# Optimization experiments

Hardware: AMD Instinct MI355X
Metric: run time of the kernel (lower is better)

## Reference

```python
import jax, jax.numpy as jnp
import numpy as np
from jax import lax

NH = 4          # num_head
DIM = 512       # attention dim
VDIM = 512      # v_dim
QDIM = 1024     # q_dim
KS = 100        # loc_kernel_size -> conv width 2*KS+1
KN = 100        # loc_kernel_num
TEMP = 0.5      # temperature
BS, TS = 8, 2048


def setup_inputs() -> dict:
    key = jax.random.key(0)
    ks = jax.random.split(key, 12)
    s = 0.05
    return {
        "dec_state": jax.random.normal(ks[0], (BS, QDIM), jnp.float32),
        "enc_feat": jax.random.normal(ks[1], (BS, TS, VDIM), jnp.float32),
        "enc_len": jax.random.randint(ks[2], (BS,), TS // 2, TS + 1).astype(jnp.int32),
        "Wq": jax.random.normal(ks[3], (NH * DIM, QDIM), jnp.float32) * s,
        "bq": jnp.zeros((NH * DIM,), jnp.float32),
        "Wk": jax.random.normal(ks[4], (NH * DIM, VDIM), jnp.float32) * s,
        "bk": jnp.zeros((NH * DIM,), jnp.float32),
        "Wv": jax.random.normal(ks[5], (NH * VDIM, VDIM), jnp.float32) * s,
        "bv": jnp.zeros((NH * VDIM,), jnp.float32),
        "loc_conv_w": jax.random.normal(ks[6], (KN, NH, 2 * KS + 1), jnp.float32) * s,
        "loc_proj_w": jax.random.normal(ks[7], (DIM, KN), jnp.float32) * s,
        "gen_w": jax.random.normal(ks[8], (1, DIM), jnp.float32) * s,
        "gen_b": jnp.zeros((1,), jnp.float32),
        "merge_w": jax.random.normal(ks[9], (VDIM, NH * VDIM), jnp.float32) * s,
        "merge_b": jnp.zeros((VDIM,), jnp.float32),
    }


def reference(dec_state, enc_feat, enc_len, Wq, bq, Wk, bk, Wv, bv,
              loc_conv_w, loc_proj_w, gen_w, gen_b, merge_w, merge_b):
    bs, ts, _ = enc_feat.shape
    # query: [bs, nh, dim]
    query = jnp.tanh(dec_state @ Wq.T + bq).reshape(bs, NH, DIM)
    # key/value: [bs, nh, ts, dim]/[bs, nh, ts, v_dim]
    key = jnp.tanh(enc_feat @ Wk.T + bk).reshape(bs, ts, NH, DIM).transpose(0, 2, 1, 3)
    value = jnp.tanh(enc_feat @ Wv.T + bv).reshape(bs, ts, NH, VDIM).transpose(0, 2, 1, 3)
    # mask & initial (uniform-over-valid) previous attention
    pos = jnp.arange(ts)
    pad_mask = pos[None, :] >= enc_len[:, None]                      # [bs, ts] True = padded
    prev = jnp.where(pad_mask, 0.0, 1.0 / enc_len[:, None].astype(jnp.float32))  # [bs, ts]
    prev_att = jnp.broadcast_to(prev[:, None, :], (bs, NH, ts))      # [bs, nh, ts]
    # location features: Conv1d(nh -> kn, width 2*KS+1, pad KS, no bias)
    conv = lax.conv_general_dilated(prev_att, loc_conv_w, (1,), [(KS, KS)],
                                    dimension_numbers=("NCH", "OIH", "NCH"))  # [bs, kn, ts]
    loc = jnp.tanh(jnp.einsum("bkt,dk->btd", conv, loc_proj_w))      # [bs, ts, dim]
    # additive energy: gen_energy(tanh(k + q + loc))
    e = jnp.tanh(key + query[:, :, None, :] + loc[:, None, :, :])    # [bs, nh, ts, dim]
    energy = jnp.einsum("bhtd,d->bht", e, gen_w[0]) + gen_b[0]
    energy = energy / TEMP
    energy = jnp.where(pad_mask[:, None, :], -jnp.inf, energy)
    attn = jax.nn.softmax(energy, axis=-1)                           # [bs, nh, ts]
    ctx = jnp.einsum("bht,bhtv->bhv", attn, value).reshape(bs, NH * VDIM)
    context = ctx @ merge_w.T + merge_b                              # [bs, v_dim]
    return attn, context
```

## Files before the change

kernel.cpp:

```cpp
#include <hip/hip_runtime.h>
#include <math.h>

#define NH 4
#define DIM 512
#define VDIM 512
#define QDIM 1024
#define KS 100
#define KN 100
#define TEMPERATURE 0.5f
#define BS 8
#define TS 2048
#define NHD (NH * DIM)

#define WS_QUERY  0
#define WS_QTAB   16384
#define WS_ENERGY 119808
#define WS_CTX    185344
#define WS_LOCI   201728
#define WS_P      205824
#define WS_F32_END 226028

typedef __bf16 bf16x8 __attribute__((ext_vector_type(8)));
typedef __bf16 bf16x4 __attribute__((ext_vector_type(4)));
typedef float  f32x4  __attribute__((ext_vector_type(4)));

#define AS1(p) ((const __attribute__((address_space(1))) void*)(p))
#define AS3(p) ((__attribute__((address_space(3))) void*)(p))

__device__ __forceinline__ float fast_tanh(float x) {
    float xc = fminf(fmaxf(x, -9.0f), 9.0f);
    float e = __expf(2.0f * xc);
    return __fdividef(e - 1.0f, e + 1.0f);
}

#define NE4 (BS * TS * VDIM / 4)
#define NW4 (NHD * VDIM / 4)
__global__ void k_cvt3(const float* __restrict__ enc, const float* __restrict__ Wk,
                       const float* __restrict__ Wv, __bf16* __restrict__ enc_bf,
                       __bf16* __restrict__ wk_bf, __bf16* __restrict__ wv_bf) {
    int i = blockIdx.x * blockDim.x + threadIdx.x;
    const float* src; __bf16* dst; int k;
    if (i < NE4)                { src = enc; dst = enc_bf; k = i; }
    else if (i < NE4 + NW4)     { src = Wk;  dst = wk_bf;  k = i - NE4; }
    else                        { src = Wv;  dst = wv_bf;  k = i - NE4 - NW4; }
    float4 v = ((const float4*)src)[k];
    bf16x4 o;
    o[0] = (__bf16)v.x; o[1] = (__bf16)v.y; o[2] = (__bf16)v.z; o[3] = (__bf16)v.w;
    ((bf16x4*)dst)[k] = o;
}

__global__ void k_query(const float* __restrict__ dec, const float* __restrict__ Wq,
                        const float* __restrict__ bq, float* __restrict__ query) {
    int w = (blockIdx.x * blockDim.x + threadIdx.x) >> 6;
    int lane = threadIdx.x & 63;
    int b = w >> 11;
    int o = w & 2047;
    const float* dr = dec + b * QDIM;
    const float* wr = Wq + o * QDIM;
    float s = 0.f;
    #pragma unroll
    for (int i = 0; i < QDIM / 64; ++i) s = fmaf(dr[lane + 64 * i], wr[lane + 64 * i], s);
    #pragma unroll
    for (int off = 32; off > 0; off >>= 1) s += __shfl_down(s, off);
    if (lane == 0) query[b * NHD + o] = tanhf(s + bq[o]);
}

__global__ void k_prefix(const float* __restrict__ convw, float* __restrict__ P) {
    int k = threadIdx.x;
    if (k >= KN) return;
    const float* wr = convw + k * (NH * (2 * KS + 1));
    float acc = 0.f;
    P[k] = 0.f;
    for (int dt = 0; dt < 2 * KS + 1; ++dt) {
        acc += wr[dt] + wr[201 + dt] + wr[402 + dt] + wr[603 + dt];
        P[(dt + 1) * KN + k] = acc;
    }
}

__global__ void k_qtab(const float* __restrict__ P, const float* __restrict__ projw,
                       float* __restrict__ Qtab) {
    int j = blockIdx.x;
    __shared__ float Pc[KN];
    int tid = threadIdx.x;
    if (tid < KN) Pc[tid] = P[j * KN + tid];
    __syncthreads();
    const float* pr = projw + tid * KN;
    float s = 0.f;
    #pragma unroll 4
    for (int k = 0; k < KN; ++k) s = fmaf(pr[k], Pc[k], s);
    Qtab[j * DIM + tid] = s;
}

__global__ void k_locI(const float* __restrict__ Qtab, const int* __restrict__ enc_len,
                       float* __restrict__ locI) {
    int idx = blockIdx.x * blockDim.x + threadIdx.x;
    int b = idx >> 9, d = idx & (DIM - 1);
    float inv_len = 1.0f / (float)enc_len[b];
    locI[idx] = fast_tanh((Qtab[(2 * KS + 1) * DIM + d] - Qtab[d]) * inv_len);
}

#define STAGE2(AshB, BshB, k0)                                                    \
    {                                                                             \
        int cch = (lane & 7) ^ (lane >> 3);                                       \
        _Pragma("unroll")                                                         \
        for (int q = 0; q < 2; ++q) {                                             \
            int slotbase = (w * 2 + q) * 64;                                      \
            int m = (slotbase >> 3) + (lane >> 3);                                \
            __builtin_amdgcn_global_load_lds(                                     \
                AS1(Abase + (size_t)m * VDIM + (k0) + cch * 8),                   \
                AS3((AshB) + slotbase * 8), 16, 0, 0);                            \
            __builtin_amdgcn_global_load_lds(                                     \
                AS1(Bbase + (size_t)m * VDIM + (k0) + cch * 8),                   \
                AS3((BshB) + slotbase * 8), 16, 0, 0);                            \
        }                                                                         \
    }

#define GEMM_MAIN(Bglobal, EARLY)                                                 \
    const int t0 = blockIdx.x * 128;                                              \
    const int n0 = blockIdx.y * 128;                                              \
    const int b  = blockIdx.z;                                                    \
    EARLY                                                                         \
    const int tid = threadIdx.x;                                                  \
    const int w = tid >> 6, lane = tid & 63;                                      \
    const int wy = w >> 2, wx = w & 3;                                            \
    const int col = lane & 15, quad = lane >> 4;                                  \
    __shared__ __bf16 Ash[2][128 * 64];                                           \
    __shared__ __bf16 Bsh[2][128 * 64];                                           \
    f32x4 acc[4][2];                                                              \
    _Pragma("unroll")                                                             \
    for (int i = 0; i < 4; ++i)                                                   \
        _Pragma("unroll")                                                         \
        for (int j = 0; j < 2; ++j) acc[i][j] = (f32x4)0.f;                       \
    const __bf16* Abase = enc_bf + ((size_t)b * TS + t0) * VDIM;                  \
    const __bf16* Bbase = (Bglobal) + (size_t)n0 * VDIM;                          \
    STAGE2(Ash[0], Bsh[0], 0)                                                     \
    for (int kk = 0; kk < 8; ++kk) {                                              \
        __syncthreads();                                                          \
        if (kk < 7) STAGE2(Ash[(kk + 1) & 1], Bsh[(kk + 1) & 1], (kk + 1) * 64)   \
        const __bf16* As = Ash[kk & 1];                                           \
        const __bf16* Bs = Bsh[kk & 1];                                           \
        _Pragma("unroll")                                                         \
        for (int ks = 0; ks < 2; ++ks) {                                          \
            bf16x8 af[4], bfr[2];                                                 \
            int jslot = ((ks * 4 + quad) ^ (col & 7));                            \
            _Pragma("unroll")                                                     \
            for (int i = 0; i < 4; ++i) {                                         \
                int m = wy * 64 + i * 16 + col;                                   \
                af[i] = *(const bf16x8*)(As + (m * 8 + jslot) * 8);               \
            }                                                                     \
            _Pragma("unroll")                                                     \
            for (int j = 0; j < 2; ++j) {                                         \
                int n = wx * 32 + j * 16 + col;                                   \
                bfr[j] = *(const bf16x8*)(Bs + (n * 8 + jslot) * 8);              \
            }                                                                     \
            _Pragma("unroll")                                                     \
            for (int i = 0; i < 4; ++i)                                           \
                _Pragma("unroll")                                                 \
                for (int j = 0; j < 2; ++j)                                       \
                    acc[i][j] = __builtin_amdgcn_mfma_f32_16x16x32_bf16(          \
                        af[i], bfr[j], acc[i][j], 0, 0, 0);                       \
        }                                                                         \
    }                                                                             \
    __syncthreads();

__global__ __launch_bounds__(512, 4) void k_energy(
    const __bf16* __restrict__ enc_bf, const __bf16* __restrict__ wk_bf,
    const float* __restrict__ bk, const float* __restrict__ gen_w,
    const int* __restrict__ enc_len, const float* __restrict__ query,
    const float* __restrict__ Qtab, const float* __restrict__ locI,
    float* __restrict__ energy) {
    GEMM_MAIN(wk_bf, const int len = enc_len[b]; if (t0 >= len) return;)

    const int h = n0 >> 9;
    const float inv_len = 1.0f / (float)len;
    float qv[2], gw[2], bkv[2], lI[2];
    int dj[2];
    #pragma unroll
    for (int j = 0; j < 2; ++j) {
        int n = n0 + wx * 32 + j * 16 + col;
        dj[j] = n & (DIM - 1);
        qv[j] = query[b * NHD + n];
        gw[j] = gen_w[dj[j]];
        bkv[j] = bk[n];
        lI[j] = locI[b * DIM + dj[j]];
    }
    float* red = (float*)Ash;
    #pragma unroll
    for (int i = 0; i < 4; ++i) {
        #pragma unroll
        for (int r = 0; r < 4; ++r) {
            int tl = wy * 64 + i * 16 + quad * 4 + r;
            int t = t0 + tl;
            float l[2];
            if (t >= KS && t < len - KS) {
                #pragma unroll
                for (int j = 0; j < 2; ++j) l[j] = lI[j];
            } else {
                int lo = KS - t; if (lo < 0) lo = 0;
                int hi = KS - t + len - 1; if (hi > 2 * KS) hi = 2 * KS;
                bool has = (hi >= lo);
                #pragma unroll
                for (int j = 0; j < 2; ++j) {
                    float cv = has
                        ? (Qtab[(hi + 1) * DIM + dj[j]] - Qtab[lo * DIM + dj[j]]) * inv_len
                        : 0.f;
                    l[j] = fast_tanh(cv);
                }
            }
            float s = 0.f;
            #pragma unroll
            for (int j = 0; j < 2; ++j) {
                float key = fast_tanh(acc[i][j][r] + bkv[j]);
                float e = fast_tanh(key + qv[j] + l[j]);
                s = fmaf(e, gw[j], s);
            }
            s += __shfl_xor(s, 1); s += __shfl_xor(s, 2);
            s += __shfl_xor(s, 4); s += __shfl_xor(s, 8);
            if (col == 0) red[tl * 4 + wx] = s;
        }
    }
    __syncthreads();
    if (tid < 128) {
        float s = red[tid * 4] + red[tid * 4 + 1] + red[tid * 4 + 2] + red[tid * 4 + 3];
        atomicAdd(&energy[(size_t)(b * NH + h) * TS + t0 + tid], s);
    }
}

__global__ void k_softmax(const float* __restrict__ energy, const int* __restrict__ enc_len,
                          const float* __restrict__ gen_b, float* __restrict__ attn) {
    int bh = blockIdx.x;
    int b = bh >> 2;
    int len = enc_len[b];
    int tid = threadIdx.x;
    int w = tid >> 6, lane = tid & 63;
    const float gb = gen_b[0];
    float ev[4];
    float mx = -INFINITY;
    #pragma unroll
    for (int i = 0; i < 4; ++i) {
        int t = i * 512 + tid;
        float e = (t < len) ? (energy[(size_t)bh * TS + t] + gb) * (1.0f / TEMPERATURE)
                            : -INFINITY;
        ev[i] = e;
        mx = fmaxf(mx, e);
    }
    __shared__ float sred[8], ssum[8];
    #pragma unroll
    for (int off = 32; off > 0; off >>= 1) mx = fmaxf(mx, __shfl_xor(mx, off));
    if (lane == 0) sred[w] = mx;
    __syncthreads();
    #pragma unroll
    for (int k = 0; k < 8; ++k) mx = fmaxf(mx, sred[k]);
    float ls = 0.f;
    #pragma unroll
    for (int i = 0; i < 4; ++i) {
        float ex = __expf(ev[i] - mx);
        ev[i] = ex;
        ls += ex;
    }
    #pragma unroll
    for (int off = 32; off > 0; off >>= 1) ls += __shfl_xor(ls, off);
    if (lane == 0) ssum[w] = ls;
    __syncthreads();
    float tot = 0.f;
    #pragma unroll
    for (int k = 0; k < 8; ++k) tot += ssum[k];
    float inv = 1.0f / tot;
    #pragma unroll
    for (int i = 0; i < 4; ++i)
        attn[(size_t)bh * TS + i * 512 + tid] = ev[i] * inv;
}

__global__ __launch_bounds__(512, 4) void k_ctx(
    const __bf16* __restrict__ enc_bf, const __bf16* __restrict__ wv_bf,
    const float* __restrict__ bv, const float* __restrict__ attn,
    const int* __restrict__ enc_len, float* __restrict__ ctx) {
    GEMM_MAIN(wv_bf, const int len = enc_len[b]; if (t0 >= len) return;)

    const int h = n0 >> 9;
    float att[4][4];
    #pragma unroll
    for (int i = 0; i < 4; ++i)
        #pragma unroll
        for (int r = 0; r < 4; ++r)
            att[i][r] = attn[(size_t)(b * NH + h) * TS + t0 + wy * 64 + i * 16 + quad * 4 + r];
    float* red = (float*)Ash;
    #pragma unroll
    for (int j = 0; j < 2; ++j) {
        int nl = wx * 32 + j * 16 + col;
        float bvn = bv[n0 + nl];
        float s = 0.f;
        #pragma unroll
        for (int i = 0; i < 4; ++i)
            #pragma unroll
            for (int r = 0; r < 4; ++r)
                s = fmaf(att[i][r], fast_tanh(acc[i][j][r] + bvn), s);
        s += __shfl_xor(s, 16); s += __shfl_xor(s, 32);
        if (quad == 0) red[nl * 2 + wy] = s;
    }
    __syncthreads();
    if (tid < 128) {
        float s = red[tid * 2] + red[tid * 2 + 1];
        atomicAdd(&ctx[(size_t)b * NHD + n0 + tid], s);
    }
}

__global__ void k_merge(const float* __restrict__ ctx, const float* __restrict__ mw,
                        const float* __restrict__ mb, float* __restrict__ out) {
    int w = (blockIdx.x * blockDim.x + threadIdx.x) >> 6;
    int lane = threadIdx.x & 63;
    int b = w >> 9;
    int o = w & 511;
    const float* c = ctx + (size_t)b * NHD;
    const float* wr = mw + (size_t)o * NHD;
    float s = 0.f;
    #pragma unroll
    for (int i = 0; i < NHD / 64; ++i) s = fmaf(c[lane + 64 * i], wr[lane + 64 * i], s);
    #pragma unroll
    for (int off = 32; off > 0; off >>= 1) s += __shfl_down(s, off);
    if (lane == 0) out[b * VDIM + o] = s + mb[o];
}

extern "C" void kernel_launch(void* const* d_in, const int* in_sizes, int n_in,
                              void* d_out, int out_size, void* d_ws, size_t ws_size,
                              hipStream_t stream) {
    const float* dec     = (const float*)d_in[0];
    const float* enc     = (const float*)d_in[1];
    const int*   enc_len = (const int*)d_in[2];
    const float* Wq      = (const float*)d_in[3];
    const float* bq      = (const float*)d_in[4];
    const float* Wk      = (const float*)d_in[5];
    const float* bk      = (const float*)d_in[6];
    const float* Wv      = (const float*)d_in[7];
    const float* bv      = (const float*)d_in[8];
    const float* convw   = (const float*)d_in[9];
    const float* projw   = (const float*)d_in[10];
    const float* gen_w   = (const float*)d_in[11];
    const float* gen_b   = (const float*)d_in[12];
    const float* merge_w = (const float*)d_in[13];
    const float* merge_b = (const float*)d_in[14];

    float* out   = (float*)d_out;
    float* ws    = (float*)d_ws;
    float* query = ws + WS_QUERY;
    float* Qtab  = ws + WS_QTAB;
    float* energy= ws + WS_ENERGY;
    float* ctx   = ws + WS_CTX;
    float* locI  = ws + WS_LOCI;
    float* Pws   = ws + WS_P;
    __bf16* enc_bf = (__bf16*)((char*)d_ws + (size_t)WS_F32_END * 4);
    __bf16* wk_bf  = enc_bf + (size_t)BS * TS * VDIM;
    __bf16* wv_bf  = wk_bf + (size_t)NHD * VDIM;

    hipMemsetAsync(energy, 0, (65536 + 16384) * sizeof(float), stream);

    k_cvt3<<<dim3((NE4 + 2 * NW4) / 256), dim3(256), 0, stream>>>(
        enc, Wk, Wv, enc_bf, wk_bf, wv_bf);
    k_query<<<dim3(BS * NHD / 4), dim3(256), 0, stream>>>(dec, Wq, bq, query);
    k_prefix<<<dim3(1), dim3(128), 0, stream>>>(convw, Pws);
    k_qtab<<<dim3(2 * KS + 2), dim3(512), 0, stream>>>(Pws, projw, Qtab);
    k_locI<<<dim3(BS * DIM / 256), dim3(256), 0, stream>>>(Qtab, enc_len, locI);
    k_energy<<<dim3(TS / 128, NHD / 128, BS), dim3(512), 0, stream>>>(
        enc_bf, wk_bf, bk, gen_w, enc_len, query, Qtab, locI, energy);
    k_softmax<<<dim3(BS * NH), dim3(512), 0, stream>>>(energy, enc_len, gen_b, out);
    k_ctx<<<dim3(TS / 128, NHD / 128, BS), dim3(512), 0, stream>>>(
        enc_bf, wv_bf, bv, out, enc_len, ctx);
    k_merge<<<dim3(BS * VDIM / 4), dim3(256), 0, stream>>>(ctx, merge_w, merge_b, out + 65536);
}
```

Baseline: 348.1 us.

## Fuse value GEMM into energy kernel and materialize bf16 value for context

Replaces the 64-wide K-step GEMM core with a 32-wide K-step core that can compute the key and value projections in the same pass, sharing the encoder tile loads. When the workspace is large enough, the fused kernel writes tanh(value) as bf16 to a buffer, and a simple weighted-sum kernel then forms the context instead of redoing the value GEMM. This avoids a second pass over enc_feat and the value GEMM after softmax, but adds a 64 MB bf16 value write and read plus scattered 2-byte stores. It also doubles the accumulator registers in the fused kernel.

```diff
diff --git a/kernel.cpp b/kernel.cpp
--- a/kernel.cpp
+++ b/kernel.cpp
@@ -19,6 +19,7 @@
 #define WS_LOCI   201728
 #define WS_P      205824
 #define WS_F32_END 226028
+#define WS_NEED_BIG (WS_F32_END * 4ull + 2ull * (8388608 + 1048576 + 1048576 + 33554432))
 
 typedef __bf16 bf16x8 __attribute__((ext_vector_type(8)));
 typedef __bf16 bf16x4 __attribute__((ext_vector_type(4)));
@@ -99,81 +100,83 @@
     locI[idx] = fast_tanh((Qtab[(2 * KS + 1) * DIM + d] - Qtab[d]) * inv_len);
 }
 
-#define STAGE2(AshB, BshB, k0)                                                    \
-    {                                                                             \
-        int cch = (lane & 7) ^ (lane >> 3);                                       \
-        _Pragma("unroll")                                                         \
-        for (int q = 0; q < 2; ++q) {                                             \
-            int slotbase = (w * 2 + q) * 64;                                      \
-            int m = (slotbase >> 3) + (lane >> 3);                                \
-            __builtin_amdgcn_global_load_lds(                                     \
-                AS1(Abase + (size_t)m * VDIM + (k0) + cch * 8),                   \
-                AS3((AshB) + slotbase * 8), 16, 0, 0);                            \
-            __builtin_amdgcn_global_load_lds(                                     \
-                AS1(Bbase + (size_t)m * VDIM + (k0) + cch * 8),                   \
-                AS3((BshB) + slotbase * 8), 16, 0, 0);                            \
-        }                                                                         \
-    }
-
-#define GEMM_MAIN(Bglobal, EARLY)                                                 \
-    const int t0 = blockIdx.x * 128;                                              \
-    const int n0 = blockIdx.y * 128;                                              \
-    const int b  = blockIdx.z;                                                    \
-    EARLY                                                                         \
-    const int tid = threadIdx.x;                                                  \
-    const int w = tid >> 6, lane = tid & 63;                                      \
-    const int wy = w >> 2, wx = w & 3;                                            \
-    const int col = lane & 15, quad = lane >> 4;                                  \
-    __shared__ __bf16 Ash[2][128 * 64];                                           \
-    __shared__ __bf16 Bsh[2][128 * 64];                                           \
-    f32x4 acc[4][2];                                                              \
-    _Pragma("unroll")                                                             \
-    for (int i = 0; i < 4; ++i)                                                   \
-        _Pragma("unroll")                                                         \
-        for (int j = 0; j < 2; ++j) acc[i][j] = (f32x4)0.f;                       \
-    const __bf16* Abase = enc_bf + ((size_t)b * TS + t0) * VDIM;                  \
-    const __bf16* Bbase = (Bglobal) + (size_t)n0 * VDIM;                          \
-    STAGE2(Ash[0], Bsh[0], 0)                                                     \
-    for (int kk = 0; kk < 8; ++kk) {                                              \
-        __syncthreads();                                                          \
-        if (kk < 7) STAGE2(Ash[(kk + 1) & 1], Bsh[(kk + 1) & 1], (kk + 1) * 64)   \
-        const __bf16* As = Ash[kk & 1];                                           \
-        const __bf16* Bs = Bsh[kk & 1];                                           \
-        _Pragma("unroll")                                                         \
-        for (int ks = 0; ks < 2; ++ks) {                                          \
-            bf16x8 af[4], bfr[2];                                                 \
-            int jslot = ((ks * 4 + quad) ^ (col & 7));                            \
-            _Pragma("unroll")                                                     \
-            for (int i = 0; i < 4; ++i) {                                         \
-                int m = wy * 64 + i * 16 + col;                                   \
-                af[i] = *(const bf16x8*)(As + (m * 8 + jslot) * 8);               \
-            }                                                                     \
-            _Pragma("unroll")                                                     \
-            for (int j = 0; j < 2; ++j) {                                         \
-                int n = wx * 32 + j * 16 + col;                                   \
-                bfr[j] = *(const bf16x8*)(Bs + (n * 8 + jslot) * 8);              \
-            }                                                                     \
-            _Pragma("unroll")                                                     \
-            for (int i = 0; i < 4; ++i)                                           \
-                _Pragma("unroll")                                                 \
-                for (int j = 0; j < 2; ++j)                                       \
-                    acc[i][j] = __builtin_amdgcn_mfma_f32_16x16x32_bf16(          \
-                        af[i], bfr[j], acc[i][j], 0, 0, 0);                       \
-        }                                                                         \
-    }                                                                             \
-    __syncthreads();
-
-__global__ __launch_bounds__(512, 4) void k_energy(
+#define GEMM32(B1ptr, B2ptr, DOV)                                                  \
+    const int t0 = blockIdx.x * 128;                                                \
+    const int n0 = blockIdx.y * 128;                                                \
+    const int b  = blockIdx.z;                                                      \
+    const int len = enc_len[b];                                                     \
+    if (t0 >= len) return;                                                          \
+    const int tid = threadIdx.x;                                                    \
+    const int w = tid >> 6, lane = tid & 63;                                        \
+    const int wy = w >> 2, wx = w & 3;                                              \
+    const int col = lane & 15, quad = lane >> 4;                                    \
+    __shared__ __bf16 Ash[2 * 4096];                                                \
+    __shared__ __bf16 B1sh[2 * 4096];                                               \
+    __shared__ __bf16 B2sh[2 * 4096];                                               \
+    f32x4 acc1[4][2], acc2[4][2];                                                   \
+    _Pragma("unroll")                                                               \
+    for (int i = 0; i < 4; ++i)                                                     \
+        _Pragma("unroll")                                                           \
+        for (int j = 0; j < 2; ++j) { acc1[i][j] = (f32x4)0.f; acc2[i][j] = (f32x4)0.f; } \
+    const __bf16* Abase = enc_bf + ((size_t)b * TS + t0) * VDIM;                    \
+    const int sm = tid >> 2;                                                        \
+    const int sj = (tid & 3) ^ (sm & 3) ^ ((sm >> 2) & 3);                          \
+    const __bf16* gpA = Abase + (size_t)sm * VDIM + sj * 8;                         \
+    const __bf16* gp1 = (B1ptr) + ((size_t)n0 + sm) * VDIM + sj * 8;                \
+    const __bf16* gp2 = (B2ptr) + ((size_t)n0 + sm) * VDIM + sj * 8;                \
+    const int cfr = quad ^ (col & 3) ^ ((col >> 2) & 3);                            \
+    const char* pA = (const char*)Ash  + (((wy * 64 + col) * 4 + cfr) << 4);        \
+    const char* p1 = (const char*)B1sh + (((wx * 32 + col) * 4 + cfr) << 4);        \
+    const char* p2 = (const char*)B2sh + (((wx * 32 + col) * 4 + cfr) << 4);        \
+    __builtin_amdgcn_global_load_lds(AS1(gpA), AS3(Ash + w * 512), 16, 0, 0);       \
+    __builtin_amdgcn_global_load_lds(AS1(gp1), AS3(B1sh + w * 512), 16, 0, 0);      \
+    if (DOV) __builtin_amdgcn_global_load_lds(AS1(gp2), AS3(B2sh + w * 512), 16, 0, 0); \
+    gpA += 32; gp1 += 32; gp2 += 32;                                                \
+    for (int kk = 0; kk < 16; ++kk) {                                               \
+        __syncthreads();                                                            \
+        if (kk < 15) {                                                              \
+            int nb = ((kk + 1) & 1) * 4096;                                         \
+            __builtin_amdgcn_global_load_lds(AS1(gpA), AS3(Ash + nb + w * 512), 16, 0, 0);  \
+            __builtin_amdgcn_global_load_lds(AS1(gp1), AS3(B1sh + nb + w * 512), 16, 0, 0); \
+            if (DOV) __builtin_amdgcn_global_load_lds(AS1(gp2), AS3(B2sh + nb + w * 512), 16, 0, 0); \
+            gpA += 32; gp1 += 32; gp2 += 32;                                        \
+        }                                                                           \
+        const int bo = (kk & 1) * 8192;                                             \
+        bf16x8 af[4], f1[2], f2[2];                                                 \
+        _Pragma("unroll")                                                           \
+        for (int i = 0; i < 4; ++i) af[i] = *(const bf16x8*)(pA + bo + i * 1024);   \
+        _Pragma("unroll")                                                           \
+        for (int j = 0; j < 2; ++j) f1[j] = *(const bf16x8*)(p1 + bo + j * 1024);   \
+        if (DOV) {                                                                  \
+            _Pragma("unroll")                                                       \
+            for (int j = 0; j < 2; ++j) f2[j] = *(const bf16x8*)(p2 + bo + j * 1024); \
+        }                                                                           \
+        _Pragma("unroll")                                                           \
+        for (int i = 0; i < 4; ++i) {                                               \
+            _Pragma("unroll")                                                       \
+            for (int j = 0; j < 2; ++j) {                                           \
+                acc1[i][j] = __builtin_amdgcn_mfma_f32_16x16x32_bf16(               \
+                    af[i], f1[j], acc1[i][j], 0, 0, 0);                             \
+                if (DOV) acc2[i][j] = __builtin_amdgcn_mfma_f32_16x16x32_bf16(      \
+                    af[i], f2[j], acc2[i][j], 0, 0, 0);                             \
+            }                                                                       \
+        }                                                                           \
+    }                                                                               \
+    __syncthreads();
+
+template<bool WITHV>
+__global__ __launch_bounds__(512, 4) void k_fused(
     const __bf16* __restrict__ enc_bf, const __bf16* __restrict__ wk_bf,
-    const float* __restrict__ bk, const float* __restrict__ gen_w,
+    const __bf16* __restrict__ wv_bf, const float* __restrict__ bk,
+    const float* __restrict__ bv, const float* __restrict__ gen_w,
     const int* __restrict__ enc_len, const float* __restrict__ query,
     const float* __restrict__ Qtab, const float* __restrict__ locI,
-    float* __restrict__ energy) {
-    GEMM_MAIN(wk_bf, const int len = enc_len[b]; if (t0 >= len) return;)
+    float* __restrict__ energy, __bf16* __restrict__ value) {
+    GEMM32(wk_bf, wv_bf, WITHV)
 
     const int h = n0 >> 9;
     const float inv_len = 1.0f / (float)len;
-    float qv[2], gw[2], bkv[2], lI[2];
+    float qv[2], gw[2], bkv[2], lI[2], bvv[2];
     int dj[2];
     #pragma unroll
     for (int j = 0; j < 2; ++j) {
@@ -183,7 +186,9 @@
         gw[j] = gen_w[dj[j]];
         bkv[j] = bk[n];
         lI[j] = locI[b * DIM + dj[j]];
-    }
+        bvv[j] = WITHV ? bv[n] : 0.f;
+    }
+    __bf16* vb = WITHV ? (value + ((size_t)(b * NH + h) * TS) * VDIM) : nullptr;
     float* red = (float*)Ash;
     #pragma unroll
     for (int i = 0; i < 4; ++i) {
@@ -210,9 +215,12 @@
             float s = 0.f;
             #pragma unroll
             for (int j = 0; j < 2; ++j) {
-                float key = fast_tanh(acc[i][j][r] + bkv[j]);
+                float key = fast_tanh(acc1[i][j][r] + bkv[j]);
                 float e = fast_tanh(key + qv[j] + l[j]);
                 s = fmaf(e, gw[j], s);
+                if (WITHV)
+                    vb[(size_t)t * VDIM + dj[j]] =
+                        (__bf16)fast_tanh(acc2[i][j][r] + bvv[j]);
             }
             s += __shfl_xor(s, 1); s += __shfl_xor(s, 2);
             s += __shfl_xor(s, 4); s += __shfl_xor(s, 8);
@@ -223,6 +231,55 @@
     if (tid < 128) {
         float s = red[tid * 4] + red[tid * 4 + 1] + red[tid * 4 + 2] + red[tid * 4 + 3];
         atomicAdd(&energy[(size_t)(b * NH + h) * TS + t0 + tid], s);
+    }
+}
+
+__global__ void k_ctxv(const __bf16* __restrict__ value, const float* __restrict__ attn,
+                       const int* __restrict__ enc_len, float* __restrict__ ctx) {
+    const int tc = blockIdx.x * 128;
+    const int h = blockIdx.y, b = blockIdx.z;
+    if (tc >= enc_len[b]) return;
+    const int bh = b * NH + h;
+    const __bf16* vbase = value + ((size_t)bh * TS + tc) * VDIM + threadIdx.x;
+    const float* abase = attn + (size_t)bh * TS + tc;
+    float s = 0.f;
+    #pragma unroll 8
+    for (int t = 0; t < 128; ++t)
+        s = fmaf(abase[t], (float)vbase[(size_t)t * VDIM], s);
+    atomicAdd(&ctx[(size_t)b * NHD + h * VDIM + threadIdx.x], s);
+}
+
+__global__ __launch_bounds__(512, 4) void k_ctxg(
+    const __bf16* __restrict__ enc_bf, const __bf16* __restrict__ wv_bf,
+    const float* __restrict__ bv, const float* __restrict__ attn,
+    const int* __restrict__ enc_len, float* __restrict__ ctx) {
+    GEMM32(wv_bf, wv_bf, 0)
+
+    const int h = n0 >> 9;
+    float att[4][4];
+    #pragma unroll
+    for (int i = 0; i < 4; ++i)
+        #pragma unroll
+        for (int r = 0; r < 4; ++r)
+            att[i][r] = attn[(size_t)(b * NH + h) * TS + t0 + wy * 64 + i * 16 + quad * 4 + r];
+    float* red = (float*)Ash;
+    #pragma unroll
+    for (int j = 0; j < 2; ++j) {
+        int nl = wx * 32 + j * 16 + col;
+        float bvn = bv[n0 + nl];
+        float s = 0.f;
+        #pragma unroll
+        for (int i = 0; i < 4; ++i)
+            #pragma unroll
+            for (int r = 0; r < 4; ++r)
+                s = fmaf(att[i][r], fast_tanh(acc1[i][j][r] + bvn), s);
+        s += __shfl_xor(s, 16); s += __shfl_xor(s, 32);
+        if (quad == 0) red[nl * 2 + wy] = s;
+    }
+    __syncthreads();
+    if (tid < 128) {
+        float s = red[tid * 2] + red[tid * 2 + 1];
+        atomicAdd(&ctx[(size_t)b * NHD + n0 + tid], s);
     }
 }
 
@@ -269,40 +326,6 @@
     #pragma unroll
     for (int i = 0; i < 4; ++i)
         attn[(size_t)bh * TS + i * 512 + tid] = ev[i] * inv;
-}
-
-__global__ __launch_bounds__(512, 4) void k_ctx(
-    const __bf16* __restrict__ enc_bf, const __bf16* __restrict__ wv_bf,
-    const float* __restrict__ bv, const float* __restrict__ attn,
-    const int* __restrict__ enc_len, float* __restrict__ ctx) {
-    GEMM_MAIN(wv_bf, const int len = enc_len[b]; if (t0 >= len) return;)
-
-    const int h = n0 >> 9;
-    float att[4][4];
-    #pragma unroll
-    for (int i = 0; i < 4; ++i)
-        #pragma unroll
-        for (int r = 0; r < 4; ++r)
-            att[i][r] = attn[(size_t)(b * NH + h) * TS + t0 + wy * 64 + i * 16 + quad * 4 + r];
-    float* red = (float*)Ash;
-    #pragma unroll
-    for (int j = 0; j < 2; ++j) {
-        int nl = wx * 32 + j * 16 + col;
-        float bvn = bv[n0 + nl];
-        float s = 0.f;
-        #pragma unroll
-        for (int i = 0; i < 4; ++i)
-            #pragma unroll
-            for (int r = 0; r < 4; ++r)
-                s = fmaf(att[i][r], fast_tanh(acc[i][j][r] + bvn), s);
-        s += __shfl_xor(s, 16); s += __shfl_xor(s, 32);
-        if (quad == 0) red[nl * 2 + wy] = s;
-    }
-    __syncthreads();
-    if (tid < 128) {
-        float s = red[tid * 2] + red[tid * 2 + 1];
-        atomicAdd(&ctx[(size_t)b * NHD + n0 + tid], s);
-    }
 }
 
 __global__ void k_merge(const float* __restrict__ ctx, const float* __restrict__ mw,
@@ -351,6 +374,8 @@
     __bf16* enc_bf = (__bf16*)((char*)d_ws + (size_t)WS_F32_END * 4);
     __bf16* wk_bf  = enc_bf + (size_t)BS * TS * VDIM;
     __bf16* wv_bf  = wk_bf + (size_t)NHD * VDIM;
+    __bf16* value  = wv_bf + (size_t)NHD * VDIM;
+    const bool big = ws_size >= WS_NEED_BIG;
 
     hipMemsetAsync(energy, 0, (65536 + 16384) * sizeof(float), stream);
 
@@ -360,10 +385,20 @@
     k_prefix<<<dim3(1), dim3(128), 0, stream>>>(convw, Pws);
     k_qtab<<<dim3(2 * KS + 2), dim3(512), 0, stream>>>(Pws, projw, Qtab);
     k_locI<<<dim3(BS * DIM / 256), dim3(256), 0, stream>>>(Qtab, enc_len, locI);
-    k_energy<<<dim3(TS / 128, NHD / 128, BS), dim3(512), 0, stream>>>(
-        enc_bf, wk_bf, bk, gen_w, enc_len, query, Qtab, locI, energy);
-    k_softmax<<<dim3(BS * NH), dim3(512), 0, stream>>>(energy, enc_len, gen_b, out);
-    k_ctx<<<dim3(TS / 128, NHD / 128, BS), dim3(512), 0, stream>>>(
-        enc_bf, wv_bf, bv, out, enc_len, ctx);
+    if (big) {
+        k_fused<true><<<dim3(TS / 128, NHD / 128, BS), dim3(512), 0, stream>>>(
+            enc_bf, wk_bf, wv_bf, bk, bv, gen_w, enc_len, query, Qtab, locI,
+            energy, value);
+        k_softmax<<<dim3(BS * NH), dim3(512), 0, stream>>>(energy, enc_len, gen_b, out);
+        k_ctxv<<<dim3(TS / 128, NH, BS), dim3(512), 0, stream>>>(
+            value, out, enc_len, ctx);
+    } else {
+        k_fused<false><<<dim3(TS / 128, NHD / 128, BS), dim3(512), 0, stream>>>(
+            enc_bf, wk_bf, wv_bf, bk, bv, gen_w, enc_len, query, Qtab, locI,
+            energy, nullptr);
+        k_softmax<<<dim3(BS * NH), dim3(512), 0, stream>>>(energy, enc_len, gen_b, out);
+        k_ctxg<<<dim3(TS / 128, NHD / 128, BS), dim3(512), 0, stream>>>(
+            enc_bf, wv_bf, bv, out, enc_len, ctx);
+    }
     k_merge<<<dim3(BS * VDIM / 4), dim3(256), 0, stream>>>(ctx, merge_w, merge_b, out + 65536);
 }
```

After: 375.5 us. 7.9% more time.

## Merge prologue kernels, inline locI, reshape GEMM K-tile and block order

Applied to the files above, without the earlier changes.

Merges the bf16 conversion, query projection and conv-prefix kernels into one launch, and computes the locI term inside the energy epilogue, so two launches and one kernel go away. The shared GEMM body now uses 32-wide K steps (16 iterations) with a new XOR swizzle and precomputed LDS pointers, which halves the LDS footprint per stage. The grid is a flattened 1D index that groups blocks of the same batch and time tile, aiming for better L2 reuse of encoder rows. The cost is twice as many barriers per GEMM and redundant tanh work for locI in every block.

```diff
diff --git a/kernel.cpp b/kernel.cpp
--- a/kernel.cpp
+++ b/kernel.cpp
@@ -16,9 +16,8 @@
 #define WS_QTAB   16384
 #define WS_ENERGY 119808
 #define WS_CTX    185344
-#define WS_LOCI   201728
-#define WS_P      205824
-#define WS_F32_END 226028
+#define WS_P      201728
+#define WS_F32_END 221928
 
 typedef __bf16 bf16x8 __attribute__((ext_vector_type(8)));
 typedef __bf16 bf16x4 __attribute__((ext_vector_type(4)));
@@ -35,45 +34,50 @@
 
 #define NE4 (BS * TS * VDIM / 4)
 #define NW4 (NHD * VDIM / 4)
-__global__ void k_cvt3(const float* __restrict__ enc, const float* __restrict__ Wk,
-                       const float* __restrict__ Wv, __bf16* __restrict__ enc_bf,
-                       __bf16* __restrict__ wk_bf, __bf16* __restrict__ wv_bf) {
-    int i = blockIdx.x * blockDim.x + threadIdx.x;
-    const float* src; __bf16* dst; int k;
-    if (i < NE4)                { src = enc; dst = enc_bf; k = i; }
-    else if (i < NE4 + NW4)     { src = Wk;  dst = wk_bf;  k = i - NE4; }
-    else                        { src = Wv;  dst = wv_bf;  k = i - NE4 - NW4; }
-    float4 v = ((const float4*)src)[k];
-    bf16x4 o;
-    o[0] = (__bf16)v.x; o[1] = (__bf16)v.y; o[2] = (__bf16)v.z; o[3] = (__bf16)v.w;
-    ((bf16x4*)dst)[k] = o;
-}
-
-__global__ void k_query(const float* __restrict__ dec, const float* __restrict__ Wq,
-                        const float* __restrict__ bq, float* __restrict__ query) {
-    int w = (blockIdx.x * blockDim.x + threadIdx.x) >> 6;
-    int lane = threadIdx.x & 63;
-    int b = w >> 11;
-    int o = w & 2047;
-    const float* dr = dec + b * QDIM;
-    const float* wr = Wq + o * QDIM;
-    float s = 0.f;
-    #pragma unroll
-    for (int i = 0; i < QDIM / 64; ++i) s = fmaf(dr[lane + 64 * i], wr[lane + 64 * i], s);
-    #pragma unroll
-    for (int off = 32; off > 0; off >>= 1) s += __shfl_down(s, off);
-    if (lane == 0) query[b * NHD + o] = tanhf(s + bq[o]);
-}
-
-__global__ void k_prefix(const float* __restrict__ convw, float* __restrict__ P) {
-    int k = threadIdx.x;
-    if (k >= KN) return;
-    const float* wr = convw + k * (NH * (2 * KS + 1));
-    float acc = 0.f;
-    P[k] = 0.f;
-    for (int dt = 0; dt < 2 * KS + 1; ++dt) {
-        acc += wr[dt] + wr[201 + dt] + wr[402 + dt] + wr[603 + dt];
-        P[(dt + 1) * KN + k] = acc;
+#define NCVT ((NE4 + 2 * NW4) / 256)
+#define NQRY (BS * NHD / 4)
+__global__ void k_precvt(const float* __restrict__ enc, const float* __restrict__ Wk,
+                         const float* __restrict__ Wv, __bf16* __restrict__ enc_bf,
+                         __bf16* __restrict__ wk_bf, __bf16* __restrict__ wv_bf,
+                         const float* __restrict__ dec, const float* __restrict__ Wq,
+                         const float* __restrict__ bq, float* __restrict__ query,
+                         const float* __restrict__ convw, float* __restrict__ P) {
+    if (blockIdx.x < NCVT) {
+        int i = blockIdx.x * blockDim.x + threadIdx.x;
+        const float* src; __bf16* dst; int k;
+        if (i < NE4)            { src = enc; dst = enc_bf; k = i; }
+        else if (i < NE4 + NW4) { src = Wk;  dst = wk_bf;  k = i - NE4; }
+        else                    { src = Wv;  dst = wv_bf;  k = i - NE4 - NW4; }
+        float4 v = ((const float4*)src)[k];
+        bf16x4 o;
+        o[0] = (__bf16)v.x; o[1] = (__bf16)v.y; o[2] = (__bf16)v.z; o[3] = (__bf16)v.w;
+        ((bf16x4*)dst)[k] = o;
+    } else if (blockIdx.x < NCVT + NQRY) {
+        int q = blockIdx.x - NCVT;
+        int w = q * 4 + (threadIdx.x >> 6);
+        int lane = threadIdx.x & 63;
+        int b = w >> 11;
+        int o = w & 2047;
+        const float* dr = dec + b * QDIM;
+        const float* wr = Wq + o * QDIM;
+        float s = 0.f;
+        #pragma unroll
+        for (int i = 0; i < QDIM / 64; ++i)
+            s = fmaf(dr[lane + 64 * i], wr[lane + 64 * i], s);
+        #pragma unroll
+        for (int off = 32; off > 0; off >>= 1) s += __shfl_down(s, off);
+        if (lane == 0) query[b * NHD + o] = tanhf(s + bq[o]);
+    } else {
+        int k = threadIdx.x;
+        if (k < KN) {
+            const float* wr = convw + k * (NH * (2 * KS + 1));
+            float acc = 0.f;
+            P[k] = 0.f;
+            for (int dt = 0; dt < 2 * KS + 1; ++dt) {
+                acc += wr[dt] + wr[201 + dt] + wr[402 + dt] + wr[603 + dt];
+                P[(dt + 1) * KN + k] = acc;
+            }
+        }
     }
 }
 
@@ -91,85 +95,64 @@
     Qtab[j * DIM + tid] = s;
 }
 
-__global__ void k_locI(const float* __restrict__ Qtab, const int* __restrict__ enc_len,
-                       float* __restrict__ locI) {
-    int idx = blockIdx.x * blockDim.x + threadIdx.x;
-    int b = idx >> 9, d = idx & (DIM - 1);
-    float inv_len = 1.0f / (float)enc_len[b];
-    locI[idx] = fast_tanh((Qtab[(2 * KS + 1) * DIM + d] - Qtab[d]) * inv_len);
-}
-
-#define STAGE2(AshB, BshB, k0)                                                    \
-    {                                                                             \
-        int cch = (lane & 7) ^ (lane >> 3);                                       \
-        _Pragma("unroll")                                                         \
-        for (int q = 0; q < 2; ++q) {                                             \
-            int slotbase = (w * 2 + q) * 64;                                      \
-            int m = (slotbase >> 3) + (lane >> 3);                                \
-            __builtin_amdgcn_global_load_lds(                                     \
-                AS1(Abase + (size_t)m * VDIM + (k0) + cch * 8),                   \
-                AS3((AshB) + slotbase * 8), 16, 0, 0);                            \
-            __builtin_amdgcn_global_load_lds(                                     \
-                AS1(Bbase + (size_t)m * VDIM + (k0) + cch * 8),                   \
-                AS3((BshB) + slotbase * 8), 16, 0, 0);                            \
-        }                                                                         \
-    }
-
-#define GEMM_MAIN(Bglobal, EARLY)                                                 \
-    const int t0 = blockIdx.x * 128;                                              \
-    const int n0 = blockIdx.y * 128;                                              \
-    const int b  = blockIdx.z;                                                    \
-    EARLY                                                                         \
-    const int tid = threadIdx.x;                                                  \
-    const int w = tid >> 6, lane = tid & 63;                                      \
-    const int wy = w >> 2, wx = w & 3;                                            \
-    const int col = lane & 15, quad = lane >> 4;                                  \
-    __shared__ __bf16 Ash[2][128 * 64];                                           \
-    __shared__ __bf16 Bsh[2][128 * 64];                                           \
-    f32x4 acc[4][2];                                                              \
-    _Pragma("unroll")                                                             \
-    for (int i = 0; i < 4; ++i)                                                   \
-        _Pragma("unroll")                                                         \
-        for (int j = 0; j < 2; ++j) acc[i][j] = (f32x4)0.f;                       \
-    const __bf16* Abase = enc_bf + ((size_t)b * TS + t0) * VDIM;                  \
-    const __bf16* Bbase = (Bglobal) + (size_t)n0 * VDIM;                          \
-    STAGE2(Ash[0], Bsh[0], 0)                                                     \
-    for (int kk = 0; kk < 8; ++kk) {                                              \
-        __syncthreads();                                                          \
-        if (kk < 7) STAGE2(Ash[(kk + 1) & 1], Bsh[(kk + 1) & 1], (kk + 1) * 64)   \
-        const __bf16* As = Ash[kk & 1];                                           \
-        const __bf16* Bs = Bsh[kk & 1];                                           \
-        _Pragma("unroll")                                                         \
-        for (int ks = 0; ks < 2; ++ks) {                                          \
-            bf16x8 af[4], bfr[2];                                                 \
-            int jslot = ((ks * 4 + quad) ^ (col & 7));                            \
-            _Pragma("unroll")                                                     \
-            for (int i = 0; i < 4; ++i) {                                         \
-                int m = wy * 64 + i * 16 + col;                                   \
-                af[i] = *(const bf16x8*)(As + (m * 8 + jslot) * 8);               \
-            }                                                                     \
-            _Pragma("unroll")                                                     \
-            for (int j = 0; j < 2; ++j) {                                         \
-                int n = wx * 32 + j * 16 + col;                                   \
-                bfr[j] = *(const bf16x8*)(Bs + (n * 8 + jslot) * 8);              \
-            }                                                                     \
-            _Pragma("unroll")                                                     \
-            for (int i = 0; i < 4; ++i)                                           \
-                _Pragma("unroll")                                                 \
-                for (int j = 0; j < 2; ++j)                                       \
-                    acc[i][j] = __builtin_amdgcn_mfma_f32_16x16x32_bf16(          \
-                        af[i], bfr[j], acc[i][j], 0, 0, 0);                       \
-        }                                                                         \
-    }                                                                             \
+#define GEMM1(Bptr)                                                               \
+    const int bid = blockIdx.x;                                                    \
+    const int b   = bid >> 8;                                                      \
+    const int t0  = ((bid >> 4) & 15) << 7;                                        \
+    const int n0  = ((((bid >> 3) & 1) << 3) | (bid & 7)) << 7;                    \
+    const int len = enc_len[b];                                                    \
+    if (t0 >= len) return;                                                         \
+    const int tid = threadIdx.x;                                                   \
+    const int w = tid >> 6, lane = tid & 63;                                       \
+    const int wy = w >> 2, wx = w & 3;                                             \
+    const int col = lane & 15, quad = lane >> 4;                                   \
+    __shared__ __bf16 Ash[2 * 4096];                                               \
+    __shared__ __bf16 Bsh[2 * 4096];                                               \
+    f32x4 acc[4][2];                                                               \
+    _Pragma("unroll")                                                              \
+    for (int i = 0; i < 4; ++i)                                                    \
+        _Pragma("unroll")                                                          \
+        for (int j = 0; j < 2; ++j) acc[i][j] = (f32x4)0.f;                        \
+    const __bf16* Abase = enc_bf + ((size_t)b * TS + t0) * VDIM;                   \
+    const int sm = tid >> 2;                                                       \
+    const int sj = (tid & 3) ^ (sm & 3) ^ ((sm >> 2) & 3);                         \
+    const __bf16* gpA = Abase + (size_t)sm * VDIM + sj * 8;                        \
+    const __bf16* gpB = (Bptr) + ((size_t)n0 + sm) * VDIM + sj * 8;                \
+    const int cfr = quad ^ (col & 3) ^ ((col >> 2) & 3);                           \
+    const char* pA = (const char*)Ash + (((wy * 64 + col) * 4 + cfr) << 4);        \
+    const char* pB = (const char*)Bsh + (((wx * 32 + col) * 4 + cfr) << 4);        \
+    __builtin_amdgcn_global_load_lds(AS1(gpA), AS3(Ash + w * 512), 16, 0, 0);      \
+    __builtin_amdgcn_global_load_lds(AS1(gpB), AS3(Bsh + w * 512), 16, 0, 0);      \
+    gpA += 32; gpB += 32;                                                          \
+    for (int kk = 0; kk < 16; ++kk) {                                              \
+        __syncthreads();                                                           \
+        if (kk < 15) {                                                             \
+            int nb_ = ((kk + 1) & 1) * 4096;                                       \
+            __builtin_amdgcn_global_load_lds(AS1(gpA), AS3(Ash + nb_ + w * 512), 16, 0, 0); \
+            __builtin_amdgcn_global_load_lds(AS1(gpB), AS3(Bsh + nb_ + w * 512), 16, 0, 0); \
+            gpA += 32; gpB += 32;                                                  \
+        }                                                                          \
+        const int bo = (kk & 1) * 8192;                                            \
+        bf16x8 af[4], bfr[2];                                                      \
+        _Pragma("unroll")                                                          \
+        for (int i = 0; i < 4; ++i) af[i] = *(const bf16x8*)(pA + bo + i * 1024);  \
+        _Pragma("unroll")                                                          \
+        for (int j = 0; j < 2; ++j) bfr[j] = *(const bf16x8*)(pB + bo + j * 1024); \
+        _Pragma("unroll")                                                          \
+        for (int i = 0; i < 4; ++i)                                                \
+            _Pragma("unroll")                                                      \
+            for (int j = 0; j < 2; ++j)                                            \
+                acc[i][j] = __builtin_amdgcn_mfma_f32_16x16x32_bf16(               \
+                    af[i], bfr[j], acc[i][j], 0, 0, 0);                            \
+    }                                                                              \
     __syncthreads();
 
 __global__ __launch_bounds__(512, 4) void k_energy(
     const __bf16* __restrict__ enc_bf, const __bf16* __restrict__ wk_bf,
     const float* __restrict__ bk, const float* __restrict__ gen_w,
     const int* __restrict__ enc_len, const float* __restrict__ query,
-    const float* __restrict__ Qtab, const float* __restrict__ locI,
-    float* __restrict__ energy) {
-    GEMM_MAIN(wk_bf, const int len = enc_len[b]; if (t0 >= len) return;)
+    const float* __restrict__ Qtab, float* __restrict__ energy) {
+    GEMM1(wk_bf)
 
     const int h = n0 >> 9;
     const float inv_len = 1.0f / (float)len;
@@ -182,7 +165,7 @@
         qv[j] = query[b * NHD + n];
         gw[j] = gen_w[dj[j]];
         bkv[j] = bk[n];
-        lI[j] = locI[b * DIM + dj[j]];
+        lI[j] = fast_tanh((Qtab[(2 * KS + 1) * DIM + dj[j]] - Qtab[dj[j]]) * inv_len);
     }
     float* red = (float*)Ash;
     #pragma unroll
@@ -226,6 +209,40 @@
     }
 }
 
+__global__ __launch_bounds__(512, 4) void k_ctxg(
+    const __bf16* __restrict__ enc_bf, const __bf16* __restrict__ wv_bf,
+    const float* __restrict__ bv, const float* __restrict__ attn,
+    const int* __restrict__ enc_len, float* __restrict__ ctx) {
+    GEMM1(wv_bf)
+
+    const int h = n0 >> 9;
+    float att[4][4];
+    #pragma unroll
+    for (int i = 0; i < 4; ++i)
+        #pragma unroll
+        for (int r = 0; r < 4; ++r)
+            att[i][r] = attn[(size_t)(b * NH + h) * TS + t0 + wy * 64 + i * 16 + quad * 4 + r];
+    float* red = (float*)Ash;
+    #pragma unroll
+    for (int j = 0; j < 2; ++j) {
+        int nl = wx * 32 + j * 16 + col;
+        float bvn = bv[n0 + nl];
+        float s = 0.f;
+        #pragma unroll
+        for (int i = 0; i < 4; ++i)
+            #pragma unroll
+            for (int r = 0; r < 4; ++r)
+                s = fmaf(att[i][r], fast_tanh(acc[i][j][r] + bvn), s);
+        s += __shfl_xor(s, 16); s += __shfl_xor(s, 32);
+        if (quad == 0) red[nl * 2 + wy] = s;
+    }
+    __syncthreads();
+    if (tid < 128) {
+        float s = red[tid * 2] + red[tid * 2 + 1];
+        atomicAdd(&ctx[(size_t)b * NHD + n0 + tid], s);
+    }
+}
+
 __global__ void k_softmax(const float* __restrict__ energy, const int* __restrict__ enc_len,
                           const float* __restrict__ gen_b, float* __restrict__ attn) {
     int bh = blockIdx.x;
@@ -269,40 +286,6 @@
     #pragma unroll
     for (int i = 0; i < 4; ++i)
         attn[(size_t)bh * TS + i * 512 + tid] = ev[i] * inv;
-}
-
-__global__ __launch_bounds__(512, 4) void k_ctx(
-    const __bf16* __restrict__ enc_bf, const __bf16* __restrict__ wv_bf,
-    const float* __restrict__ bv, const float* __restrict__ attn,
-    const int* __restrict__ enc_len, float* __restrict__ ctx) {
-    GEMM_MAIN(wv_bf, const int len = enc_len[b]; if (t0 >= len) return;)
-
-    const int h = n0 >> 9;
-    float att[4][4];
-    #pragma unroll
-    for (int i = 0; i < 4; ++i)
-        #pragma unroll
-        for (int r = 0; r < 4; ++r)
-            att[i][r] = attn[(size_t)(b * NH + h) * TS + t0 + wy * 64 + i * 16 + quad * 4 + r];
-    float* red = (float*)Ash;
-    #pragma unroll
-    for (int j = 0; j < 2; ++j) {
-        int nl = wx * 32 + j * 16 + col;
-        float bvn = bv[n0 + nl];
-        float s = 0.f;
-        #pragma unroll
-        for (int i = 0; i < 4; ++i)
-            #pragma unroll
-            for (int r = 0; r < 4; ++r)
-                s = fmaf(att[i][r], fast_tanh(acc[i][j][r] + bvn), s);
-        s += __shfl_xor(s, 16); s += __shfl_xor(s, 32);
-        if (quad == 0) red[nl * 2 + wy] = s;
-    }
-    __syncthreads();
-    if (tid < 128) {
-        float s = red[tid * 2] + red[tid * 2 + 1];
-        atomicAdd(&ctx[(size_t)b * NHD + n0 + tid], s);
-    }
 }
 
 __global__ void k_merge(const float* __restrict__ ctx, const float* __restrict__ mw,
@@ -346,7 +329,6 @@
     float* Qtab  = ws + WS_QTAB;
     float* energy= ws + WS_ENERGY;
     float* ctx   = ws + WS_CTX;
-    float* locI  = ws + WS_LOCI;
     float* Pws   = ws + WS_P;
     __bf16* enc_bf = (__bf16*)((char*)d_ws + (size_t)WS_F32_END * 4);
     __bf16* wk_bf  = enc_bf + (size_t)BS * TS * VDIM;
@@ -354,16 +336,13 @@
 
     hipMemsetAsync(energy, 0, (65536 + 16384) * sizeof(float), stream);
 
-    k_cvt3<<<dim3((NE4 + 2 * NW4) / 256), dim3(256), 0, stream>>>(
-        enc, Wk, Wv, enc_bf, wk_bf, wv_bf);
-    k_query<<<dim3(BS * NHD / 4), dim3(256), 0, stream>>>(dec, Wq, bq, query);
-    k_prefix<<<dim3(1), dim3(128), 0, stream>>>(convw, Pws);
+    k_precvt<<<dim3(NCVT + NQRY + 1), dim3(256), 0, stream>>>(
+        enc, Wk, Wv, enc_bf, wk_bf, wv_bf, dec, Wq, bq, query, convw, Pws);
     k_qtab<<<dim3(2 * KS + 2), dim3(512), 0, stream>>>(Pws, projw, Qtab);
-    k_locI<<<dim3(BS * DIM / 256), dim3(256), 0, stream>>>(Qtab, enc_len, locI);
-    k_energy<<<dim3(TS / 128, NHD / 128, BS), dim3(512), 0, stream>>>(
-        enc_bf, wk_bf, bk, gen_w, enc_len, query, Qtab, locI, energy);
+    k_energy<<<dim3(2048), dim3(512), 0, stream>>>(
+        enc_bf, wk_bf, bk, gen_w, enc_len, query, Qtab, energy);
     k_softmax<<<dim3(BS * NH), dim3(512), 0, stream>>>(energy, enc_len, gen_b, out);
-    k_ctx<<<dim3(TS / 128, NHD / 128, BS), dim3(512), 0, stream>>>(
+    k_ctxg<<<dim3(2048), dim3(512), 0, stream>>>(
         enc_bf, wv_bf, bv, out, enc_len, ctx);
     k_merge<<<dim3(BS * VDIM / 4), dim3(256), 0, stream>>>(ctx, merge_w, merge_b, out + 65536);
 }
```

After: 330.5 us. 5.1% less time.
